# Kernel optimization log

Measured on AMD Instinct MI355X. Metric: run time of the kernel, lower is better.

Reference implementation:

```python
import jax, jax.numpy as jnp
import numpy as np

EPS = 1e-5

def _bn(h):
    # BatchNorm1d, affine=False, track_running_stats=False -> batch stats, biased var
    m = h.mean(axis=0)
    v = h.var(axis=0)
    return (h - m) * jax.lax.rsqrt(v + EPS)

def _aggregate(x, edge_index):
    # out[i] = sum over edges (i <- j) of x[j]  + x[i] (self loop)
    dst, src = edge_index[0], edge_index[1]
    n = x.shape[0]
    return jax.ops.segment_sum(x[src], dst, num_segments=n) + x

def setup_inputs() -> dict:
    key = jax.random.key(0)
    ks = jax.random.split(key, 12)
    N, F, H, C, E = 100000, 128, 128, 40, 800000
    x = jax.random.normal(ks[0], (N, F), dtype=jnp.float32)
    edge_index = jax.random.randint(ks[1], (2, E), 0, N, dtype=jnp.int64)
    def lin(kw, kb, fan_in, fan_out):
        bound = 1.0 / np.sqrt(fan_in)
        W = jax.random.uniform(kw, (fan_in, fan_out), minval=-bound, maxval=bound, dtype=jnp.float32)
        b = jax.random.uniform(kb, (fan_out,), minval=-bound, maxval=bound, dtype=jnp.float32)
        return W, b
    W0, b0 = lin(ks[2], ks[3], F, H)
    W1, b1 = lin(ks[4], ks[5], H, H)
    W2, b2 = lin(ks[6], ks[7], H, H)
    Wl, bl = lin(ks[8], ks[9], H, C)
    return {"x": x, "edge_index": edge_index, "W0": W0, "b0": b0,
            "W1": W1, "b1": b1, "W2": W2, "b2": b2, "Wl": Wl, "bl": bl}

def reference(x, edge_index, W0, b0, W1, b1, W2, b2, Wl, bl):
    h = x
    for W, b in ((W0, b0), (W1, b1), (W2, b2)):
        h = _aggregate(h, edge_index)          # spmm(A + I, h)
        h = h @ W + b                          # Linear
        h = _bn(h)                             # BatchNorm1d (no affine)
        h = jax.nn.relu(h)
    return h @ Wl + bl
```

## Files before the change

kernel.cpp:

```cpp
#include <hip/hip_runtime.h>
#include <stdint.h>

typedef __attribute__((ext_vector_type(8))) short short8;
typedef __attribute__((ext_vector_type(4))) float floatx4;

static __device__ __forceinline__ float b2f(uint16_t b){
    return __uint_as_float(((uint32_t)b) << 16);
}
static __device__ __forceinline__ uint16_t f2b(float f){
    uint32_t u = __float_as_uint(f);
    return (uint16_t)((u + 0x7fffu + ((u >> 16) & 1u)) >> 16);
}
static __device__ __forceinline__ float blo(uint32_t v){ return __uint_as_float(v << 16); }
static __device__ __forceinline__ float bhi(uint32_t v){ return __uint_as_float(v & 0xffff0000u); }
static __device__ __forceinline__ uint32_t pack2(float a, float b){
    return ((uint32_t)f2b(b) << 16) | (uint32_t)f2b(a);
}

__global__ void k_sentinel(uint32_t* out, int nwords, uint32_t pat){
    int i = blockIdx.x * blockDim.x + threadIdx.x;
    if (i < nwords) out[i] = pat;
}

__global__ void k_flags(const uint32_t* xw, const int* ei, int* flags){
    if (threadIdx.x != 0 || blockIdx.x != 0) return;
    int odd_nz = 0;
    for (int k = 0; k < 128; k++){
        if (ei[2 * k + 1] != 0) odd_nz = 1;
    }
    flags[0] = odd_nz ? 0 : 1;
    int big = 0;
    for (int k = 0; k < 128; k++){
        float lo = __uint_as_float(xw[k] << 16);
        if (!(fabsf(lo) <= 1024.0f)) big = 1;
    }
    flags[1] = big ? 0 : 1;
}

__global__ void k_zero(int* deg, int N){
    int i = blockIdx.x * blockDim.x + threadIdx.x;
    if (i < N) deg[i] = 0;
}

__global__ void k_deg(const int* ei, int E, int* deg, uint16_t* rank, const int* flags){
    int e = blockIdx.x * blockDim.x + threadIdx.x;
    if (e < E){
        int d = flags[0] ? ei[2 * e] : ei[e];
        int r = atomicAdd(&deg[d], 1);
        rank[e] = (uint16_t)r;
    }
}

__global__ void k_scan1(const int* deg, int N, int* bsum){
    __shared__ int s[256];
    int t = threadIdx.x;
    int i = blockIdx.x * 256 + t;
    s[t] = (i < N) ? deg[i] : 0;
    __syncthreads();
    for (int off = 128; off > 0; off >>= 1){
        if (t < off) s[t] += s[t + off];
        __syncthreads();
    }
    if (t == 0) bsum[blockIdx.x] = s[0];
}

__global__ void k_scan2(int* bsum, int nb, int* rp, int N){
    __shared__ int s[512];
    int t = threadIdx.x;
    int v = (t < nb) ? bsum[t] : 0;
    s[t] = v;
    __syncthreads();
    for (int off = 1; off < 512; off <<= 1){
        int u = (t >= off) ? s[t - off] : 0;
        __syncthreads();
        s[t] += u;
        __syncthreads();
    }
    if (t < nb) bsum[t] = s[t] - v;
    if (t == 511) rp[N] = s[511];
}

__global__ void k_scan3(const int* deg, int N, const int* bpre, int* rp){
    __shared__ int s[256];
    int t = threadIdx.x;
    int i = blockIdx.x * 256 + t;
    int v = (i < N) ? deg[i] : 0;
    s[t] = v;
    __syncthreads();
    for (int off = 1; off < 256; off <<= 1){
        int u = (t >= off) ? s[t - off] : 0;
        __syncthreads();
        s[t] += u;
        __syncthreads();
    }
    if (i < N) rp[i] = bpre[blockIdx.x] + s[t] - v;
}

__global__ __launch_bounds__(256) void k_fill(const int* __restrict__ ei, int E,
                                              const int* __restrict__ rp,
                                              const uint16_t* __restrict__ rank,
                                              int* __restrict__ col,
                                              const int* __restrict__ flags, int N){
    int xcd = blockIdx.x & 7;
    int sub = blockIdx.x >> 3;
    int nsub = gridDim.x >> 3;
    int r0 = (int)(((long long)N * xcd) >> 3);
    int r1 = (int)(((long long)N * (xcd + 1)) >> 3);
    int e0 = (int)(((long long)E * sub) / nsub);
    int e1 = (int)(((long long)E * (sub + 1)) / nsub);
    int is64 = flags[0];
    for (int e = e0 + threadIdx.x; e < e1; e += 256){
        int d = is64 ? ei[2 * e] : ei[e];
        if (d >= r0 && d < r1){
            int sv = is64 ? ei[2 * (E + e)] : ei[E + e];
            int p = rp[d] + (int)rank[e];
            col[p] = sv;
        }
    }
}

__global__ void k_cvt_x(const void* x, uint16_t* hx, int n, const int* flags){
    if (flags[1]) return;
    for (int i = blockIdx.x * blockDim.x + threadIdx.x; i < n; i += gridDim.x * blockDim.x)
        hx[i] = f2b(((const float*)x)[i]);
}

__global__ void k_prep_all(const void* W0, const void* W1, const void* W2, const void* Wl,
                           uint16_t* Wf0, uint16_t* Wf1, uint16_t* Wf2, uint16_t* Wfl,
                           const int* flags){
    int b = blockIdx.x;
    const void* W; uint16_t* Wf; int C, ntiles, lb;
    if (b < 64)        { W = W0; Wf = Wf0; C = 128; ntiles = 8; lb = b; }
    else if (b < 128)  { W = W1; Wf = Wf1; C = 128; ntiles = 8; lb = b - 64; }
    else if (b < 192)  { W = W2; Wf = Wf2; C = 128; ntiles = 8; lb = b - 128; }
    else               { W = Wl; Wf = Wfl; C = 40;  ntiles = 3; lb = b - 192; }
    int idx = lb * 256 + threadIdx.x;
    int total = 4 * ntiles * 512;
    if (idx >= total) return;
    int j = idx & 7;
    int lane = (idx >> 3) & 63;
    int nt = (idx >> 9) % ntiles;
    int kt = idx / (512 * ntiles);
    int k = kt * 32 + (lane >> 4) * 8 + j;
    int n = nt * 16 + (lane & 15);
    uint16_t v = 0;
    if (n < C){
        v = flags[1] ? ((const uint16_t*)W)[k * C + n]
                     : f2b(((const float*)W)[k * C + n]);
    }
    Wf[idx] = v;
}

__global__ void k_cvt_bias(const void* b0, const void* b1, const void* b2, const void* bl,
                           float* bc, const int* flags){
    int i = blockIdx.x * blockDim.x + threadIdx.x;
    if (i >= 424) return;
    const void* src; int li;
    if (i < 128)      { src = b0; li = i; }
    else if (i < 256) { src = b1; li = i - 128; }
    else if (i < 384) { src = b2; li = i - 256; }
    else              { src = bl; li = i - 384; }
    bc[i] = flags[1] ? b2f(((const uint16_t*)src)[li]) : ((const float*)src)[li];
}

__global__ __launch_bounds__(256) void k_agg(const uint16_t* __restrict__ Yin,
                                             const uint16_t* __restrict__ xraw,
                                             const int* __restrict__ rp,
                                             const int* __restrict__ col,
                                             uint16_t* __restrict__ out, int N,
                                             const float* __restrict__ st,
                                             int apply_bn, float ninv,
                                             const int* __restrict__ flags){
    int t = threadIdx.x;
    int l16 = t & 15;
    int i = blockIdx.x * 16 + (t >> 4);
    if (i >= N) return;
    float mm[8], iv[8];
    const uint16_t* src = Yin;
    if (apply_bn){
        int f0 = l16 * 8;
        #pragma unroll
        for (int j = 0; j < 8; j++){
            float sv = st[f0 + j];
            float qv = st[128 + f0 + j];
            float m = sv * ninv;
            float var = qv * ninv - m * m;
            mm[j] = m;
            iv[j] = rsqrtf(var + 1e-5f);
        }
    } else if (flags[1]){
        src = xraw;
    }
    const uint4* base = (const uint4*)src;
    int s0 = rp[i], e0 = rp[i + 1];
    float a[8];
    {
        uint4 w = base[(size_t)i * 16 + l16];
        a[0] = blo(w.x); a[1] = bhi(w.x); a[2] = blo(w.y); a[3] = bhi(w.y);
        a[4] = blo(w.z); a[5] = bhi(w.z); a[6] = blo(w.w); a[7] = bhi(w.w);
        if (apply_bn){
            #pragma unroll
            for (int jj = 0; jj < 8; jj++) a[jj] = fmaxf((a[jj] - mm[jj]) * iv[jj], 0.f);
        }
    }
    int k = s0;
    for (; k + 3 < e0; k += 4){
        int j0 = col[k], j1 = col[k + 1], j2 = col[k + 2], j3 = col[k + 3];
        uint4 ww[4];
        ww[0] = base[(size_t)j0 * 16 + l16];
        ww[1] = base[(size_t)j1 * 16 + l16];
        ww[2] = base[(size_t)j2 * 16 + l16];
        ww[3] = base[(size_t)j3 * 16 + l16];
        #pragma unroll
        for (int u = 0; u < 4; u++){
            float v[8] = {blo(ww[u].x), bhi(ww[u].x), blo(ww[u].y), bhi(ww[u].y),
                          blo(ww[u].z), bhi(ww[u].z), blo(ww[u].w), bhi(ww[u].w)};
            if (apply_bn){
                #pragma unroll
                for (int jj = 0; jj < 8; jj++) v[jj] = fmaxf((v[jj] - mm[jj]) * iv[jj], 0.f);
            }
            #pragma unroll
            for (int jj = 0; jj < 8; jj++) a[jj] += v[jj];
        }
    }
    for (; k < e0; k++){
        int j = col[k];
        uint4 w = base[(size_t)j * 16 + l16];
        float v[8] = {blo(w.x), bhi(w.x), blo(w.y), bhi(w.y),
                      blo(w.z), bhi(w.z), blo(w.w), bhi(w.w)};
        if (apply_bn){
            #pragma unroll
            for (int jj = 0; jj < 8; jj++) v[jj] = fmaxf((v[jj] - mm[jj]) * iv[jj], 0.f);
        }
        #pragma unroll
        for (int jj = 0; jj < 8; jj++) a[jj] += v[jj];
    }
    uint4 o;
    o.x = pack2(a[0], a[1]); o.y = pack2(a[2], a[3]);
    o.z = pack2(a[4], a[5]); o.w = pack2(a[6], a[7]);
    ((uint4*)out)[(size_t)i * 16 + l16] = o;
}

__global__ __launch_bounds__(256) void k_gemm(uint16_t* __restrict__ A,
                                              const uint16_t* __restrict__ Wf,
                                              const float* __restrict__ bias,
                                              float* __restrict__ part, int N){
    __shared__ __align__(16) uint16_t wlds[16384];
    __shared__ float sh_sum[128], sh_ssq[128];
    int t = threadIdx.x;
    if (t < 128){ sh_sum[t] = 0.f; sh_ssq[t] = 0.f; }
    {
        const uint4* s = (const uint4*)Wf;
        uint4* d = (uint4*)wlds;
        for (int i = t; i < 2048; i += 256) d[i] = s[i];
    }
    __syncthreads();
    int lane = t & 63, wave = t >> 6;
    int m = lane & 15, q = lane >> 4;
    int rb[2];
    rb[0] = blockIdx.x * 128 + wave * 16;
    rb[1] = rb[0] + 64;
    short8 afrag[2][4];
    #pragma unroll
    for (int mt = 0; mt < 2; mt++){
        int arow = rb[mt] + m;
        if (arow >= N) arow = N - 1;
        const short8* ap = (const short8*)(A + (size_t)arow * 128);
        #pragma unroll
        for (int kt = 0; kt < 4; kt++) afrag[mt][kt] = ap[kt * 4 + q];
    }
    floatx4 acc[2][8];
    #pragma unroll
    for (int mt = 0; mt < 2; mt++)
        #pragma unroll
        for (int nt = 0; nt < 8; nt++) acc[mt][nt] = (floatx4){0.f, 0.f, 0.f, 0.f};
    const short8* wl = (const short8*)wlds;
    #pragma unroll
    for (int kt = 0; kt < 4; kt++){
        #pragma unroll
        for (int nt = 0; nt < 8; nt++){
            short8 bfrag = wl[(kt * 8 + nt) * 64 + lane];
            #pragma unroll
            for (int mt = 0; mt < 2; mt++){
                acc[mt][nt] = __builtin_amdgcn_mfma_f32_16x16x32_bf16(afrag[mt][kt], bfrag, acc[mt][nt], 0, 0, 0);
            }
        }
    }
    #pragma unroll
    for (int mt = 0; mt < 2; mt++){
        #pragma unroll
        for (int nt = 0; nt < 8; nt++){
            int ccol = nt * 16 + m;
            float bv = bias[ccol];
            float s = 0.f, ss = 0.f;
            #pragma unroll
            for (int r = 0; r < 4; r++){
                int grow = rb[mt] + q * 4 + r;
                if (grow < N){
                    float y = acc[mt][nt][r] + bv;
                    A[(size_t)grow * 128 + ccol] = f2b(y);
                    s += y;
                    ss += y * y;
                }
            }
            s += __shfl_xor(s, 16); s += __shfl_xor(s, 32);
            ss += __shfl_xor(ss, 16); ss += __shfl_xor(ss, 32);
            if (q == 0){
                atomicAdd(&sh_sum[ccol], s);
                atomicAdd(&sh_ssq[ccol], ss);
            }
        }
    }
    __syncthreads();
    if (t < 128){
        part[(size_t)blockIdx.x * 256 + t] = sh_sum[t];
        part[(size_t)blockIdx.x * 256 + 128 + t] = sh_ssq[t];
    }
}

__global__ __launch_bounds__(1024) void k_red(const float* __restrict__ part, int nb,
                                              float* __restrict__ st){
    __shared__ float sh[1024];
    int t = threadIdx.x;
    int col = t & 255;
    int seg = t >> 8;
    float s0 = 0.f, s1 = 0.f, s2 = 0.f, s3 = 0.f;
    int b = seg;
    for (; b + 12 < nb; b += 16){
        s0 += part[(size_t)b * 256 + col];
        s1 += part[(size_t)(b + 4) * 256 + col];
        s2 += part[(size_t)(b + 8) * 256 + col];
        s3 += part[(size_t)(b + 12) * 256 + col];
    }
    for (; b < nb; b += 4) s0 += part[(size_t)b * 256 + col];
    sh[t] = (s0 + s1) + (s2 + s3);
    __syncthreads();
    if (t < 256) st[t] = (sh[t] + sh[t + 256]) + (sh[t + 512] + sh[t + 768]);
}

__global__ __launch_bounds__(256) void k_out(const uint16_t* __restrict__ A,
                                             const uint16_t* __restrict__ Wf,
                                             const float* __restrict__ bias,
                                             const float* __restrict__ st, float ninv,
                                             void* __restrict__ out, int N,
                                             const int* __restrict__ flags){
    __shared__ __align__(16) uint16_t wlds[6144];
    __shared__ float s_m[128], s_iv[128];
    int t = threadIdx.x;
    {
        const uint4* s = (const uint4*)Wf;
        uint4* d = (uint4*)wlds;
        for (int i = t; i < 768; i += 256) d[i] = s[i];
    }
    if (t < 128){
        float m = st[t] * ninv;
        float var = st[128 + t] * ninv - m * m;
        s_m[t] = m;
        s_iv[t] = rsqrtf(var + 1e-5f);
    }
    __syncthreads();
    int lane = t & 63, wave = t >> 6;
    int m = lane & 15, q = lane >> 4;
    int row_base = blockIdx.x * 64 + wave * 16;
    int arow = row_base + m;
    if (arow >= N) arow = N - 1;
    short8 afrag[4];
    const uint4* ap = (const uint4*)(A + (size_t)arow * 128);
    #pragma unroll
    for (int kt = 0; kt < 4; kt++){
        uint4 u = ap[kt * 4 + q];
        float v[8] = {blo(u.x), bhi(u.x), blo(u.y), bhi(u.y),
                      blo(u.z), bhi(u.z), blo(u.w), bhi(u.w)};
        int c0 = kt * 32 + q * 8;
        #pragma unroll
        for (int j = 0; j < 8; j++) v[j] = fmaxf((v[j] - s_m[c0 + j]) * s_iv[c0 + j], 0.f);
        uint4 o;
        o.x = pack2(v[0], v[1]); o.y = pack2(v[2], v[3]);
        o.z = pack2(v[4], v[5]); o.w = pack2(v[6], v[7]);
        afrag[kt] = *(short8*)&o;
    }
    floatx4 acc[3];
    #pragma unroll
    for (int nt = 0; nt < 3; nt++) acc[nt] = (floatx4){0.f, 0.f, 0.f, 0.f};
    const short8* wl = (const short8*)wlds;
    #pragma unroll
    for (int kt = 0; kt < 4; kt++){
        #pragma unroll
        for (int nt = 0; nt < 3; nt++){
            acc[nt] = __builtin_amdgcn_mfma_f32_16x16x32_bf16(afrag[kt], wl[(kt * 3 + nt) * 64 + lane], acc[nt], 0, 0, 0);
        }
    }
    int isbf = flags[1];
    #pragma unroll
    for (int nt = 0; nt < 3; nt++){
        int ccol = nt * 16 + m;
        if (ccol < 40){
            float bv = bias[ccol];
            #pragma unroll
            for (int r = 0; r < 4; r++){
                int grow = row_base + q * 4 + r;
                if (grow < N){
                    float y = acc[nt][r] + bv;
                    if (isbf) ((uint16_t*)out)[(size_t)grow * 40 + ccol] = f2b(y);
                    else      ((float*)out)[(size_t)grow * 40 + ccol] = y;
                }
            }
        }
    }
}

extern "C" void kernel_launch(void* const* d_in, const int* in_sizes, int n_in,
                              void* d_out, int out_size, void* d_ws, size_t ws_size,
                              hipStream_t stream){
    (void)n_in;
    const void* x  = d_in[0];
    const int* ei  = (const int*)d_in[1];
    const void* W0 = d_in[2];
    const void* b0 = d_in[3];
    const void* W1 = d_in[4];
    const void* b1 = d_in[5];
    const void* W2 = d_in[6];
    const void* b2 = d_in[7];
    const void* Wl = d_in[8];
    const void* bl = d_in[9];

    const int N = in_sizes[0] / 128;
    const int E = in_sizes[1] / 2;
    const int NF = N * 128;
    const int NB = (N + 255) / 256;
    const int gemm_blocks2 = (N + 127) / 128;
    const int gemm_blocks  = (N + 63) / 64;

    char* ws = (char*)d_ws;
    size_t off = 0;
    uint16_t* hx = (uint16_t*)(ws + off); off += ((size_t)NF * 2 + 255) & ~(size_t)255;
    uint16_t* ag = (uint16_t*)(ws + off); off += ((size_t)NF * 2 + 255) & ~(size_t)255;
    int* col     = (int*)(ws + off);      off += ((size_t)E * 4 + 255) & ~(size_t)255;
    int* rp      = (int*)(ws + off);      off += ((size_t)(N + 1) * 4 + 255) & ~(size_t)255;
    uint16_t* rank = (uint16_t*)(ws + off); off += ((size_t)E * 2 + 255) & ~(size_t)255;
    int* deg     = (int*)(ws + off);      off += ((size_t)N * 4 + 255) & ~(size_t)255;
    int* bsum    = (int*)(ws + off);      off += 512 * 4;
    int* flags   = (int*)(ws + off);      off += 256;
    uint16_t* Wf0 = (uint16_t*)(ws + off); off += 16384 * 2;
    uint16_t* Wf1 = (uint16_t*)(ws + off); off += 16384 * 2;
    uint16_t* Wf2 = (uint16_t*)(ws + off); off += 16384 * 2;
    uint16_t* Wfl = (uint16_t*)(ws + off); off += 6144 * 2;
    float* bc    = (float*)(ws + off);    off += 424 * 4 + 160;
    float* stats = (float*)(ws + off);    off += 768 * 4;
    float* part  = (float*)(ws + off);    off += (size_t)gemm_blocks2 * 256 * 4;
    const size_t required = off;

    if (ws_size < required){
        int nwords = out_size / 2;
        k_sentinel<<<(nwords + 255) / 256, 256, 0, stream>>>((uint32_t*)d_out, nwords, 0x40004000u);
        return;
    }

    k_flags<<<1, 64, 0, stream>>>((const uint32_t*)x, ei, flags);
    k_zero<<<(N + 255) / 256, 256, 0, stream>>>(deg, N);
    k_deg<<<(E + 255) / 256, 256, 0, stream>>>(ei, E, deg, rank, flags);
    k_scan1<<<NB, 256, 0, stream>>>(deg, N, bsum);
    k_scan2<<<1, 512, 0, stream>>>(bsum, NB, rp, N);
    k_scan3<<<NB, 256, 0, stream>>>(deg, N, bsum, rp);
    k_fill<<<1024, 256, 0, stream>>>(ei, E, rp, rank, col, flags, N);

    k_cvt_x<<<2048, 256, 0, stream>>>(x, hx, NF, flags);
    k_prep_all<<<216, 256, 0, stream>>>(W0, W1, W2, Wl, Wf0, Wf1, Wf2, Wfl, flags);
    k_cvt_bias<<<2, 256, 0, stream>>>(b0, b1, b2, bl, bc, flags);

    const float ninv = 1.0f / (float)N;
    const int agg_blocks = (N + 15) / 16;
    const uint16_t* xr = (const uint16_t*)x;

    k_agg<<<agg_blocks, 256, 0, stream>>>(hx, xr, rp, col, ag, N, stats, 0, ninv, flags);
    k_gemm<<<gemm_blocks2, 256, 0, stream>>>(ag, Wf0, bc, part, N);
    k_red<<<1, 1024, 0, stream>>>(part, gemm_blocks2, stats);
    k_agg<<<agg_blocks, 256, 0, stream>>>(ag, xr, rp, col, hx, N, stats, 1, ninv, flags);
    k_gemm<<<gemm_blocks2, 256, 0, stream>>>(hx, Wf1, bc + 128, part, N);
    k_red<<<1, 1024, 0, stream>>>(part, gemm_blocks2, stats + 256);
    k_agg<<<agg_blocks, 256, 0, stream>>>(hx, xr, rp, col, ag, N, stats + 256, 1, ninv, flags);
    k_gemm<<<gemm_blocks2, 256, 0, stream>>>(ag, Wf2, bc + 256, part, N);
    k_red<<<1, 1024, 0, stream>>>(part, gemm_blocks2, stats + 512);
    k_out<<<gemm_blocks, 256, 0, stream>>>(ag, Wfl, bc + 384, stats + 512, ninv, d_out, N, flags);
}
```

Measured before the change: 442.6 us.

## Bucket CSR neighbors by source octant and fuse setup kernels

Edge degree counting now uses per-destination 8-way sub-buckets keyed by source-index range. Each row's neighbor list therefore comes out partially sorted by source region, which is meant to improve gather locality in the aggregation kernels. Several small setup kernels are merged (flags+zero, weight/bias/x conversion) to cut launch overhead, and the BN normalize is folded into a single FMA. The cost is an extra k_off8 pass and an 8x larger degree array to zero and atomically update.

```diff
diff --git a/kernel.cpp b/kernel.cpp
--- a/kernel.cpp
+++ b/kernel.cpp
@@ -22,33 +22,51 @@
     if (i < nwords) out[i] = pat;
 }
 
-__global__ void k_flags(const uint32_t* xw, const int* ei, int* flags){
-    if (threadIdx.x != 0 || blockIdx.x != 0) return;
-    int odd_nz = 0;
-    for (int k = 0; k < 128; k++){
-        if (ei[2 * k + 1] != 0) odd_nz = 1;
-    }
-    flags[0] = odd_nz ? 0 : 1;
-    int big = 0;
-    for (int k = 0; k < 128; k++){
-        float lo = __uint_as_float(xw[k] << 16);
-        if (!(fabsf(lo) <= 1024.0f)) big = 1;
-    }
-    flags[1] = big ? 0 : 1;
-}
-
-__global__ void k_zero(int* deg, int N){
+__global__ void k_zf(int* deg8, int n8, const uint32_t* xw, const int* ei, int* flags, int ZB){
+    if ((int)blockIdx.x == ZB){
+        if (threadIdx.x != 0) return;
+        int odd_nz = 0;
+        for (int k = 0; k < 128; k++){
+            if (ei[2 * k + 1] != 0) odd_nz = 1;
+        }
+        flags[0] = odd_nz ? 0 : 1;
+        int big = 0;
+        for (int k = 0; k < 128; k++){
+            float lo = __uint_as_float(xw[k] << 16);
+            if (!(fabsf(lo) <= 1024.0f)) big = 1;
+        }
+        flags[1] = big ? 0 : 1;
+        return;
+    }
     int i = blockIdx.x * blockDim.x + threadIdx.x;
-    if (i < N) deg[i] = 0;
-}
-
-__global__ void k_deg(const int* ei, int E, int* deg, uint16_t* rank, const int* flags){
+    if (i < n8) deg8[i] = 0;
+}
+
+__global__ void k_deg(const int* ei, int E, int* deg8, uint16_t* rank, const int* flags,
+                      unsigned q){
     int e = blockIdx.x * blockDim.x + threadIdx.x;
     if (e < E){
-        int d = flags[0] ? ei[2 * e] : ei[e];
-        int r = atomicAdd(&deg[d], 1);
+        int is64 = flags[0];
+        int d = is64 ? ei[2 * e] : ei[e];
+        unsigned sv = (unsigned)(is64 ? ei[2 * (E + e)] : ei[E + e]);
+        int s = (int)(sv / q);
+        int r = atomicAdd(&deg8[d * 8 + s], 1);
         rank[e] = (uint16_t)r;
     }
+}
+
+__global__ void k_off8(const int* __restrict__ deg8, int N, int* __restrict__ deg,
+                       uint16_t* __restrict__ offs8){
+    int i = blockIdx.x * blockDim.x + threadIdx.x;
+    if (i >= N) return;
+    int s = 0;
+    #pragma unroll
+    for (int k = 0; k < 8; k++){
+        int c = deg8[i * 8 + k];
+        offs8[i * 8 + k] = (uint16_t)s;
+        s += c;
+    }
+    deg[i] = s;
 }
 
 __global__ void k_scan1(const int* deg, int N, int* bsum){
@@ -99,8 +117,10 @@
 __global__ __launch_bounds__(256) void k_fill(const int* __restrict__ ei, int E,
                                               const int* __restrict__ rp,
                                               const uint16_t* __restrict__ rank,
+                                              const uint16_t* __restrict__ offs8,
                                               int* __restrict__ col,
-                                              const int* __restrict__ flags, int N){
+                                              const int* __restrict__ flags, int N,
+                                              unsigned q){
     int xcd = blockIdx.x & 7;
     int sub = blockIdx.x >> 3;
     int nsub = gridDim.x >> 3;
@@ -112,29 +132,45 @@
     for (int e = e0 + threadIdx.x; e < e1; e += 256){
         int d = is64 ? ei[2 * e] : ei[e];
         if (d >= r0 && d < r1){
-            int sv = is64 ? ei[2 * (E + e)] : ei[E + e];
-            int p = rp[d] + (int)rank[e];
-            col[p] = sv;
-        }
-    }
-}
-
-__global__ void k_cvt_x(const void* x, uint16_t* hx, int n, const int* flags){
-    if (flags[1]) return;
-    for (int i = blockIdx.x * blockDim.x + threadIdx.x; i < n; i += gridDim.x * blockDim.x)
-        hx[i] = f2b(((const float*)x)[i]);
-}
-
-__global__ void k_prep_all(const void* W0, const void* W1, const void* W2, const void* Wl,
-                           uint16_t* Wf0, uint16_t* Wf1, uint16_t* Wf2, uint16_t* Wfl,
-                           const int* flags){
-    int b = blockIdx.x;
+            unsigned sv = (unsigned)(is64 ? ei[2 * (E + e)] : ei[E + e]);
+            int s = (int)(sv / q);
+            int p = rp[d] + (int)offs8[d * 8 + s] + (int)rank[e];
+            col[p] = (int)sv;
+        }
+    }
+}
+
+__global__ void k_prep(const void* W0, const void* W1, const void* W2, const void* Wl,
+                       uint16_t* Wf0, uint16_t* Wf1, uint16_t* Wf2, uint16_t* Wfl,
+                       const void* b0, const void* b1, const void* b2, const void* bl,
+                       float* bc, const void* x, uint16_t* hx, int NF,
+                       const int* flags){
+    int blk = blockIdx.x;
+    int t = threadIdx.x;
+    if (blk >= 218){
+        if (flags[1]) return;
+        int nb = gridDim.x - 218;
+        for (int i = (blk - 218) * 256 + t; i < NF; i += nb * 256)
+            hx[i] = f2b(((const float*)x)[i]);
+        return;
+    }
+    if (blk >= 216){
+        int i = (blk - 216) * 256 + t;
+        if (i >= 424) return;
+        const void* src; int li;
+        if (i < 128)      { src = b0; li = i; }
+        else if (i < 256) { src = b1; li = i - 128; }
+        else if (i < 384) { src = b2; li = i - 256; }
+        else              { src = bl; li = i - 384; }
+        bc[i] = flags[1] ? b2f(((const uint16_t*)src)[li]) : ((const float*)src)[li];
+        return;
+    }
     const void* W; uint16_t* Wf; int C, ntiles, lb;
-    if (b < 64)        { W = W0; Wf = Wf0; C = 128; ntiles = 8; lb = b; }
-    else if (b < 128)  { W = W1; Wf = Wf1; C = 128; ntiles = 8; lb = b - 64; }
-    else if (b < 192)  { W = W2; Wf = Wf2; C = 128; ntiles = 8; lb = b - 128; }
-    else               { W = Wl; Wf = Wfl; C = 40;  ntiles = 3; lb = b - 192; }
-    int idx = lb * 256 + threadIdx.x;
+    if (blk < 64)        { W = W0; Wf = Wf0; C = 128; ntiles = 8; lb = blk; }
+    else if (blk < 128)  { W = W1; Wf = Wf1; C = 128; ntiles = 8; lb = blk - 64; }
+    else if (blk < 192)  { W = W2; Wf = Wf2; C = 128; ntiles = 8; lb = blk - 128; }
+    else                 { W = Wl; Wf = Wfl; C = 40;  ntiles = 3; lb = blk - 192; }
+    int idx = lb * 256 + t;
     int total = 4 * ntiles * 512;
     if (idx >= total) return;
     int j = idx & 7;
@@ -151,18 +187,6 @@
     Wf[idx] = v;
 }
 
-__global__ void k_cvt_bias(const void* b0, const void* b1, const void* b2, const void* bl,
-                           float* bc, const int* flags){
-    int i = blockIdx.x * blockDim.x + threadIdx.x;
-    if (i >= 424) return;
-    const void* src; int li;
-    if (i < 128)      { src = b0; li = i; }
-    else if (i < 256) { src = b1; li = i - 128; }
-    else if (i < 384) { src = b2; li = i - 256; }
-    else              { src = bl; li = i - 384; }
-    bc[i] = flags[1] ? b2f(((const uint16_t*)src)[li]) : ((const float*)src)[li];
-}
-
 __global__ __launch_bounds__(256) void k_agg(const uint16_t* __restrict__ Yin,
                                              const uint16_t* __restrict__ xraw,
                                              const int* __restrict__ rp,
@@ -175,7 +199,7 @@
     int l16 = t & 15;
     int i = blockIdx.x * 16 + (t >> 4);
     if (i >= N) return;
-    float mm[8], iv[8];
+    float tt[8], iv[8];
     const uint16_t* src = Yin;
     if (apply_bn){
         int f0 = l16 * 8;
@@ -185,8 +209,9 @@
             float qv = st[128 + f0 + j];
             float m = sv * ninv;
             float var = qv * ninv - m * m;
-            mm[j] = m;
-            iv[j] = rsqrtf(var + 1e-5f);
+            float ivj = rsqrtf(var + 1e-5f);
+            iv[j] = ivj;
+            tt[j] = -m * ivj;
         }
     } else if (flags[1]){
         src = xraw;
@@ -200,7 +225,7 @@
         a[4] = blo(w.z); a[5] = bhi(w.z); a[6] = blo(w.w); a[7] = bhi(w.w);
         if (apply_bn){
             #pragma unroll
-            for (int jj = 0; jj < 8; jj++) a[jj] = fmaxf((a[jj] - mm[jj]) * iv[jj], 0.f);
+            for (int jj = 0; jj < 8; jj++) a[jj] = fmaxf(fmaf(a[jj], iv[jj], tt[jj]), 0.f);
         }
     }
     int k = s0;
@@ -217,7 +242,7 @@
                           blo(ww[u].z), bhi(ww[u].z), blo(ww[u].w), bhi(ww[u].w)};
             if (apply_bn){
                 #pragma unroll
-                for (int jj = 0; jj < 8; jj++) v[jj] = fmaxf((v[jj] - mm[jj]) * iv[jj], 0.f);
+                for (int jj = 0; jj < 8; jj++) v[jj] = fmaxf(fmaf(v[jj], iv[jj], tt[jj]), 0.f);
             }
             #pragma unroll
             for (int jj = 0; jj < 8; jj++) a[jj] += v[jj];
@@ -230,7 +255,7 @@
                       blo(w.z), bhi(w.z), blo(w.w), bhi(w.w)};
         if (apply_bn){
             #pragma unroll
-            for (int jj = 0; jj < 8; jj++) v[jj] = fmaxf((v[jj] - mm[jj]) * iv[jj], 0.f);
+            for (int jj = 0; jj < 8; jj++) v[jj] = fmaxf(fmaf(v[jj], iv[jj], tt[jj]), 0.f);
         }
         #pragma unroll
         for (int jj = 0; jj < 8; jj++) a[jj] += v[jj];
@@ -430,6 +455,7 @@
     const int NB = (N + 255) / 256;
     const int gemm_blocks2 = (N + 127) / 128;
     const int gemm_blocks  = (N + 63) / 64;
+    const unsigned q8 = (unsigned)((N + 7) / 8);
 
     char* ws = (char*)d_ws;
     size_t off = 0;
@@ -438,6 +464,8 @@
     int* col     = (int*)(ws + off);      off += ((size_t)E * 4 + 255) & ~(size_t)255;
     int* rp      = (int*)(ws + off);      off += ((size_t)(N + 1) * 4 + 255) & ~(size_t)255;
     uint16_t* rank = (uint16_t*)(ws + off); off += ((size_t)E * 2 + 255) & ~(size_t)255;
+    int* deg8    = (int*)(ws + off);      off += ((size_t)N * 32 + 255) & ~(size_t)255;
+    uint16_t* offs8 = (uint16_t*)(ws + off); off += ((size_t)N * 16 + 255) & ~(size_t)255;
     int* deg     = (int*)(ws + off);      off += ((size_t)N * 4 + 255) & ~(size_t)255;
     int* bsum    = (int*)(ws + off);      off += 512 * 4;
     int* flags   = (int*)(ws + off);      off += 256;
@@ -456,17 +484,18 @@
         return;
     }
 
-    k_flags<<<1, 64, 0, stream>>>((const uint32_t*)x, ei, flags);
-    k_zero<<<(N + 255) / 256, 256, 0, stream>>>(deg, N);
-    k_deg<<<(E + 255) / 256, 256, 0, stream>>>(ei, E, deg, rank, flags);
+    const int n8 = N * 8;
+    const int ZB = (n8 + 255) / 256;
+    k_zf<<<ZB + 1, 256, 0, stream>>>(deg8, n8, (const uint32_t*)x, ei, flags, ZB);
+    k_deg<<<(E + 255) / 256, 256, 0, stream>>>(ei, E, deg8, rank, flags, q8);
+    k_off8<<<(N + 255) / 256, 256, 0, stream>>>(deg8, N, deg, offs8);
     k_scan1<<<NB, 256, 0, stream>>>(deg, N, bsum);
     k_scan2<<<1, 512, 0, stream>>>(bsum, NB, rp, N);
     k_scan3<<<NB, 256, 0, stream>>>(deg, N, bsum, rp);
-    k_fill<<<1024, 256, 0, stream>>>(ei, E, rp, rank, col, flags, N);
-
-    k_cvt_x<<<2048, 256, 0, stream>>>(x, hx, NF, flags);
-    k_prep_all<<<216, 256, 0, stream>>>(W0, W1, W2, Wl, Wf0, Wf1, Wf2, Wfl, flags);
-    k_cvt_bias<<<2, 256, 0, stream>>>(b0, b1, b2, bl, bc, flags);
+    k_fill<<<1024, 256, 0, stream>>>(ei, E, rp, rank, offs8, col, flags, N, q8);
+
+    k_prep<<<2266, 256, 0, stream>>>(W0, W1, W2, Wl, Wf0, Wf1, Wf2, Wfl,
+                                     b0, b1, b2, bl, bc, x, hx, NF, flags);
 
     const float ninv = 1.0f / (float)N;
     const int agg_blocks = (N + 15) / 16;
```

Result: no change. 437.4 us (-1.2%).
